# Performance work log

Measured on AMD Instinct MI355X. Metric: run time of the kernel, lower is better.

Reference implementation:

```python
import jax, jax.numpy as jnp
import numpy as np

H, DH = 16, 64  # heads, dim_head; inner = H*DH = 1024
EPS = 1e-5


def _ln(t, g, b):
    mu = jnp.mean(t, axis=-1, keepdims=True)
    var = jnp.var(t, axis=-1, keepdims=True)
    return (t - mu) * jax.lax.rsqrt(var + EPS) * g + b


def _split_heads(t):
    b, n, _ = t.shape
    return t.reshape(b, n, H, DH).transpose(0, 2, 1, 3)  # (b,h,n,dh)


def setup_inputs() -> dict:
    key = jax.random.key(0)
    ks = jax.random.split(key, 5)
    B, S, M, D = 16, 64, 4096, 1024  # S must equal DH (see source einsum quirk)
    return {
        "x": jax.random.normal(ks[0], (B, S, D), jnp.float32),
        "latents": jax.random.normal(ks[1], (B, M, D), jnp.float32),
        "ln_x_g": jnp.ones((D,), jnp.float32),
        "ln_x_b": jnp.zeros((D,), jnp.float32),
        "ln_l_g": jnp.ones((D,), jnp.float32),
        "ln_l_b": jnp.zeros((D,), jnp.float32),
        "Wq": jax.random.normal(ks[2], (D, H * DH), jnp.float32) * 0.02,
        "Wkv": jax.random.normal(ks[3], (D, 2 * H * DH), jnp.float32) * 0.02,
        "Wout": jax.random.normal(ks[4], (H * DH, D), jnp.float32) * 0.02,
    }


def reference(x, latents, ln_x_g, ln_x_b, ln_l_g, ln_l_b, Wq, Wkv, Wout):
    scale = DH ** -0.5
    xn = _ln(x, ln_x_g, ln_x_b)          # (B,S,D)
    ln = _ln(latents, ln_l_g, ln_l_b)    # (B,M,D)
    q = _split_heads(ln @ Wq) * scale    # (B,H,M,DH)
    k, v = map(_split_heads, jnp.split(xn @ Wkv, 2, axis=-1))  # (B,H,S,DH)
    sim = jnp.einsum('bhid,bhjd->bhij', q, k)                  # (B,H,M,S)
    sim = sim - jax.lax.stop_gradient(jnp.max(sim, axis=-1, keepdims=True))
    attn = jax.nn.softmax(sim, axis=-1)
    # Faithful to source: einsum('b h i d, b h j d -> b h i j', attn, v)
    # contracts attn's S dim with v's DH dim (requires S == DH); out = attn @ v^T.
    out = jnp.einsum('bhis,bhjs->bhij', attn, v)               # (B,H,M,S)
    b, _, m, _ = out.shape
    out = out.transpose(0, 2, 1, 3).reshape(b, m, H * DH)      # (B,M,inner)
    return out @ Wout                                          # (B,M,D)
```

## Files before the change

### kernel.cpp

```cpp
#include <hip/hip_runtime.h>
#include <stdint.h>

#define B_ 16
#define S_ 64
#define M_ 4096
#define D_ 1024
#define H_ 16
#define DH_ 64

typedef unsigned short ushort_t;
typedef __attribute__((ext_vector_type(8))) __bf16 bfrag;
typedef __attribute__((ext_vector_type(4))) float f32x4;

__device__ __forceinline__ ushort_t f2bf(float f) {
  union { float f; uint32_t u; } v; v.f = f;
  uint32_t r = v.u + 0x7fffu + ((v.u >> 16) & 1u);
  return (ushort_t)(r >> 16);
}

__device__ __forceinline__ void gload_lds16(const void* g, void* l) {
  __builtin_amdgcn_global_load_lds((const __attribute__((address_space(1))) void*)g,
                                   (__attribute__((address_space(3))) void*)l, 16, 0, 0);
}

__device__ __forceinline__ f32x4 mfma16x16x32(bfrag a, bfrag b, f32x4 c) {
  return __builtin_amdgcn_mfma_f32_16x16x32_bf16(a, b, c, 0, 0, 0);
}

__device__ __forceinline__ int fsw(int r) { return (((r >> 2) & 3) << 1) | (r & 1); }

__global__ __launch_bounds__(256) void ln_rows_kernel(
    const float* __restrict__ x, const float* __restrict__ g,
    const float* __restrict__ bta, ushort_t* __restrict__ out) {
  const int row = blockIdx.x;
  const int t = threadIdx.x;
  const float4* xr = (const float4*)(x + (size_t)row * D_);
  float4 v = xr[t];
  float s = v.x + v.y + v.z + v.w;
  float ss = v.x * v.x + v.y * v.y + v.z * v.z + v.w * v.w;
#pragma unroll
  for (int o = 32; o >= 1; o >>= 1) { s += __shfl_down(s, o); ss += __shfl_down(ss, o); }
  __shared__ float red[16];
  const int wid = t >> 6;
  if ((t & 63) == 0) { red[wid] = s; red[8 + wid] = ss; }
  __syncthreads();
  float tot = red[0] + red[1] + red[2] + red[3];
  float tot2 = red[8] + red[9] + red[10] + red[11];
  float mu = tot * (1.0f / D_);
  float var = tot2 * (1.0f / D_) - mu * mu;
  float rstd = rsqrtf(var + 1e-5f);
  float4 gg = ((const float4*)g)[t];
  float4 bb = ((const float4*)bta)[t];
  ushort_t ob[4];
  ob[0] = f2bf((v.x - mu) * rstd * gg.x + bb.x);
  ob[1] = f2bf((v.y - mu) * rstd * gg.y + bb.y);
  ob[2] = f2bf((v.z - mu) * rstd * gg.z + bb.z);
  ob[3] = f2bf((v.w - mu) * rstd * gg.w + bb.w);
  *(uint2*)(out + (size_t)row * D_ + t * 4) = *(const uint2*)ob;
}

__global__ void transpose_cast_kernel(const float* __restrict__ W, ushort_t* __restrict__ WT,
                                      int N, float scale) {
  __shared__ float tile[32][33];
  const int n0 = blockIdx.x * 32, k0 = blockIdx.y * 32;
  const int tx = threadIdx.x, ty = threadIdx.y;
#pragma unroll
  for (int i = ty; i < 32; i += 8)
    tile[i][tx] = W[(size_t)(k0 + i) * N + n0 + tx];
  __syncthreads();
#pragma unroll
  for (int i = ty; i < 32; i += 8)
    WT[(size_t)(n0 + i) * D_ + k0 + tx] = f2bf(tile[tx][i] * scale);
}

__global__ __launch_bounds__(256) void gemm_kv_kernel(
    const ushort_t* __restrict__ A, const ushort_t* __restrict__ Bt,
    ushort_t* __restrict__ kb, ushort_t* __restrict__ vb) {
  __shared__ __align__(16) ushort_t sA[128 * 32];
  __shared__ __align__(16) ushort_t sB[128 * 32];
  const int tid = threadIdx.x, wid = tid >> 6, lane = tid & 63;
  const size_t arow0 = (size_t)blockIdx.x * 128;
  const size_t brow0 = (size_t)blockIdx.y * 128;
  const int wr = (wid >> 1) * 64, wc = (wid & 1) * 64;
  const int srow = tid >> 2, scol = (tid & 3) * 8;
  const ushort_t* ga = A + (arow0 + srow) * (size_t)D_ + scol;
  const ushort_t* gb = Bt + (brow0 + srow) * (size_t)D_ + scol;
  const int frow = lane & 15, kslot = (lane >> 4) * 8;
  f32x4 acc[4][4] = {};
  for (int k0 = 0; k0 < D_; k0 += 32) {
    gload_lds16(ga, sA + wid * 512);
    gload_lds16(ga + 64 * (size_t)D_, sA + 2048 + wid * 512);
    gload_lds16(gb, sB + wid * 512);
    gload_lds16(gb + 64 * (size_t)D_, sB + 2048 + wid * 512);
    ga += 32; gb += 32;
    __syncthreads();
    bfrag af[4], bfv[4];
#pragma unroll
    for (int m = 0; m < 4; ++m)
      af[m] = *(const bfrag*)&sA[(wr + m * 16 + frow) * 32 + kslot];
#pragma unroll
    for (int n = 0; n < 4; ++n)
      bfv[n] = *(const bfrag*)&sB[(wc + n * 16 + frow) * 32 + kslot];
#pragma unroll
    for (int m = 0; m < 4; ++m)
#pragma unroll
      for (int n = 0; n < 4; ++n)
        acc[m][n] = mfma16x16x32(af[m], bfv[n], acc[m][n]);
    __syncthreads();
  }
  const int erow = (lane >> 4) * 4, ecol = lane & 15;
#pragma unroll
  for (int m = 0; m < 4; ++m)
#pragma unroll
    for (int n = 0; n < 4; ++n)
#pragma unroll
      for (int r = 0; r < 4; ++r) {
        size_t i = arow0 + wr + m * 16 + erow + r;
        int bb = (int)(i >> 6), s = (int)(i & 63);
        size_t n2 = brow0 + wc + n * 16 + ecol;
        ushort_t val = f2bf(acc[m][n][r]);
        ushort_t* dst = (n2 < 1024) ? kb : vb;
        size_t hh = (n2 & 1023) >> 6, d = n2 & 63;
        dst[(((size_t)bb * H_ + hh) * S_ + s) * DH_ + d] = val;
      }
}

template <int MODE>
__global__ __launch_bounds__(256, 2) void gemm128_kernel(
    const ushort_t* __restrict__ A, const ushort_t* __restrict__ Bt,
    const ushort_t* __restrict__ kbuf, const ushort_t* __restrict__ vbuf,
    void* __restrict__ Cout) {
  __shared__ __align__(16) ushort_t lds[24576];
  const int tid = threadIdx.x, wid = tid >> 6, lane = tid & 63;
  const int frow = lane & 15, klo = lane >> 4;
  const int wm = wid >> 1, wn = wid & 1;

  const int l = ((int)blockIdx.x & 7) * 256 + ((int)blockIdx.x >> 3);
  const int mblk = l >> 3, nblk = l & 7;
  const size_t arow0 = (size_t)mblk * 256;
  const size_t bcol0 = (size_t)nblk * 128;

  const int r0 = tid >> 2;
  const int gsrc = (tid & 3) ^ ((tid >> 3) & 3);
  const ushort_t* pA = A + (arow0 + r0) * (size_t)D_ + gsrc * 8;
  const ushort_t* pB = Bt + (bcol0 + r0) * (size_t)D_ + gsrc * 8;
  const int rasw = (klo ^ ((frow >> 1) & 3)) * 8;

#define STAGE(G)                                                                   \
  do {                                                                             \
    const int s_ = (G) & 1;                                                        \
    const size_t ko_ = (size_t)((G) < 32 ? (G) : 31) * 32;                         \
    gload_lds16(pA + ko_, &lds[s_ * 8192 + wid * 512]);                            \
    gload_lds16(pA + 64 * (size_t)D_ + ko_, &lds[s_ * 8192 + 2048 + wid * 512]);   \
    gload_lds16(pA + 128 * (size_t)D_ + ko_, &lds[s_ * 8192 + 4096 + wid * 512]);  \
    gload_lds16(pA + 192 * (size_t)D_ + ko_, &lds[s_ * 8192 + 6144 + wid * 512]);  \
    gload_lds16(pB + ko_, &lds[16384 + s_ * 4096 + wid * 512]);                    \
    gload_lds16(pB + 64 * (size_t)D_ + ko_, &lds[16384 + s_ * 4096 + 2048 + wid * 512]); \
  } while (0)

  STAGE(0);
  STAGE(1);

  f32x4 acc[8][4] = {};
  for (int g = 0; g < 32; ++g) {
    asm volatile("s_waitcnt vmcnt(6)" ::: "memory");
    __builtin_amdgcn_s_barrier();
    asm volatile("" ::: "memory");
    const ushort_t* As = &lds[(g & 1) * 8192];
    const ushort_t* Bs = &lds[16384 + (g & 1) * 4096];
    bfrag a_[8], b_[4];
#pragma unroll
    for (int mf = 0; mf < 8; ++mf)
      a_[mf] = *(const bfrag*)&As[(wm * 128 + mf * 16 + frow) * 32 + rasw];
#pragma unroll
    for (int nf = 0; nf < 4; ++nf)
      b_[nf] = *(const bfrag*)&Bs[(wn * 64 + nf * 16 + frow) * 32 + rasw];
    __builtin_amdgcn_s_setprio(1);
#pragma unroll
    for (int mf = 0; mf < 8; ++mf)
#pragma unroll
      for (int nf = 0; nf < 4; ++nf)
        acc[mf][nf] = mfma16x16x32(a_[mf], b_[nf], acc[mf][nf]);
    __builtin_amdgcn_s_setprio(0);
    asm volatile("" ::: "memory");
    __builtin_amdgcn_s_barrier();
    asm volatile("" ::: "memory");
    STAGE(g + 2);
  }
  asm volatile("s_waitcnt vmcnt(0)" ::: "memory");
  __builtin_amdgcn_s_barrier();
  asm volatile("" ::: "memory");
#undef STAGE

  if constexpr (MODE == 0) {
    float* C = (float*)Cout;
#pragma unroll
    for (int m = 0; m < 8; ++m)
#pragma unroll
      for (int n = 0; n < 4; ++n)
#pragma unroll
        for (int r = 0; r < 4; ++r)
          C[(arow0 + wm * 128 + m * 16 + klo * 4 + r) * 1024 + bcol0 + wn * 64 + n * 16 + frow] =
              acc[m][n][r];
  } else {
    ushort_t* W = &lds[wid * 4096];
    ushort_t* out1 = (ushort_t*)Cout;
    const int head = nblk * 2 + wn;
    const int bbatch = mblk >> 4;
    const size_t kvbase = ((size_t)bbatch * H_ + head) * (size_t)(S_ * DH_);
    bfrag kb[4][2], vb[4][2];
#pragma unroll
    for (int nf = 0; nf < 4; ++nf)
#pragma unroll
      for (int kk = 0; kk < 2; ++kk) {
        kb[nf][kk] = *(const bfrag*)&kbuf[kvbase + (nf * 16 + frow) * 64 + kk * 32 + klo * 8];
        vb[nf][kk] = *(const bfrag*)&vbuf[kvbase + (nf * 16 + frow) * 64 + kk * 32 + klo * 8];
      }
#pragma unroll
    for (int hh = 0; hh < 2; ++hh) {
#pragma unroll
      for (int m2 = 0; m2 < 4; ++m2)
#pragma unroll
        for (int r = 0; r < 4; ++r) {
          const int row = m2 * 16 + klo * 4 + r;
          const int fs = fsw(row);
#pragma unroll
          for (int n = 0; n < 4; ++n) {
            const int cc = n * 16 + frow;
            W[row * 64 + ((((cc >> 3) ^ fs) << 3) | (cc & 7))] = f2bf(acc[hh * 4 + m2][n][r]);
          }
        }
      f32x4 s[4][4] = {};
#pragma unroll
      for (int m2 = 0; m2 < 4; ++m2) {
        const int row = m2 * 16 + frow;
        const int fs = fsw(row);
#pragma unroll
        for (int kk = 0; kk < 2; ++kk) {
          bfrag qa = *(const bfrag*)&W[row * 64 + (((kk * 4 + klo) ^ fs) << 3)];
#pragma unroll
          for (int nf = 0; nf < 4; ++nf)
            s[m2][nf] = mfma16x16x32(qa, kb[nf][kk], s[m2][nf]);
        }
      }
#pragma unroll
      for (int m2 = 0; m2 < 4; ++m2)
#pragma unroll
        for (int r = 0; r < 4; ++r) {
          float a0 = s[m2][0][r], a1 = s[m2][1][r], a2 = s[m2][2][r], a3 = s[m2][3][r];
          float mx = fmaxf(fmaxf(a0, a1), fmaxf(a2, a3));
#pragma unroll
          for (int o = 1; o < 16; o <<= 1) mx = fmaxf(mx, __shfl_xor(mx, o));
          a0 = __expf(a0 - mx); a1 = __expf(a1 - mx);
          a2 = __expf(a2 - mx); a3 = __expf(a3 - mx);
          float sm = (a0 + a1) + (a2 + a3);
#pragma unroll
          for (int o = 1; o < 16; o <<= 1) sm += __shfl_xor(sm, o);
          const float inv = 1.0f / sm;
          s[m2][0][r] = a0 * inv; s[m2][1][r] = a1 * inv;
          s[m2][2][r] = a2 * inv; s[m2][3][r] = a3 * inv;
        }
#pragma unroll
      for (int m2 = 0; m2 < 4; ++m2)
#pragma unroll
        for (int r = 0; r < 4; ++r) {
          const int row = m2 * 16 + klo * 4 + r;
          const int fs = fsw(row);
#pragma unroll
          for (int n = 0; n < 4; ++n) {
            const int cc = n * 16 + frow;
            W[row * 64 + ((((cc >> 3) ^ fs) << 3) | (cc & 7))] = f2bf(s[m2][n][r]);
          }
        }
      f32x4 o[4][4] = {};
#pragma unroll
      for (int m2 = 0; m2 < 4; ++m2) {
        const int row = m2 * 16 + frow;
        const int fs = fsw(row);
#pragma unroll
        for (int kk = 0; kk < 2; ++kk) {
          bfrag pa = *(const bfrag*)&W[row * 64 + (((kk * 4 + klo) ^ fs) << 3)];
#pragma unroll
          for (int nf = 0; nf < 4; ++nf)
            o[m2][nf] = mfma16x16x32(pa, vb[nf][kk], o[m2][nf]);
        }
      }
#pragma unroll
      for (int m2 = 0; m2 < 4; ++m2)
#pragma unroll
        for (int r = 0; r < 4; ++r) {
          const int row = m2 * 16 + klo * 4 + r;
          const int fs = fsw(row);
#pragma unroll
          for (int n = 0; n < 4; ++n) {
            const int cc = n * 16 + frow;
            W[row * 64 + ((((cc >> 3) ^ fs) << 3) | (cc & 7))] = f2bf(o[m2][n][r]);
          }
        }
      const size_t grow0 = arow0 + wm * 128 + hh * 64;
#pragma unroll
      for (int it = 0; it < 8; ++it) {
        const int idx = it * 64 + lane;
        const int rr = idx >> 3, gs = idx & 7;
        const int gcol = (gs ^ fsw(rr)) << 3;
        *(uint4*)&out1[(grow0 + rr) * 1024 + head * 64 + gcol] =
            *(const uint4*)&W[rr * 64 + gs * 8];
      }
    }
  }
}

extern "C" void kernel_launch(void* const* d_in, const int* in_sizes, int n_in,
                              void* d_out, int out_size, void* d_ws, size_t ws_size,
                              hipStream_t stream) {
  const float* x = (const float*)d_in[0];
  const float* lat = (const float*)d_in[1];
  const float* lxg = (const float*)d_in[2];
  const float* lxb = (const float*)d_in[3];
  const float* llg = (const float*)d_in[4];
  const float* llb = (const float*)d_in[5];
  const float* Wq = (const float*)d_in[6];
  const float* Wkv = (const float*)d_in[7];
  const float* Wout = (const float*)d_in[8];
  float* out = (float*)d_out;
  char* ws = (char*)d_ws;

  ushort_t* xn = (ushort_t*)(ws);
  ushort_t* wqT = (ushort_t*)(ws + (2ull << 20));
  ushort_t* wkvT = (ushort_t*)(ws + (4ull << 20));
  ushort_t* woT = (ushort_t*)(ws + (8ull << 20));
  ushort_t* kbuf = (ushort_t*)(ws + (10ull << 20));
  ushort_t* vbuf = (ushort_t*)(ws + (12ull << 20));
  ushort_t* out1 = (ushort_t*)(ws + (14ull << 20));
  ushort_t* lnl = (ushort_t*)d_out;

  dim3 tb(32, 8);
  transpose_cast_kernel<<<dim3(1024 / 32, 32), tb, 0, stream>>>(Wq, wqT, 1024, 0.125f);
  transpose_cast_kernel<<<dim3(2048 / 32, 32), tb, 0, stream>>>(Wkv, wkvT, 2048, 1.0f);
  transpose_cast_kernel<<<dim3(1024 / 32, 32), tb, 0, stream>>>(Wout, woT, 1024, 1.0f);
  ln_rows_kernel<<<B_ * S_, 256, 0, stream>>>(x, lxg, lxb, xn);
  ln_rows_kernel<<<B_ * M_, 256, 0, stream>>>(lat, llg, llb, lnl);
  gemm_kv_kernel<<<dim3(8, 16), 256, 0, stream>>>(xn, wkvT, kbuf, vbuf);
  gemm128_kernel<1><<<2048, 256, 0, stream>>>(lnl, wqT, kbuf, vbuf, out1);
  gemm128_kernel<0><<<2048, 256, 0, stream>>>(out1, woT, nullptr, nullptr, out);
}
```

Baseline: 501.3 us.

## Shrink GEMM tiles to 128x128 and drop double-buffered LDS pipeline

Replaces the 256x128 double-buffered GEMM with a 128x128 single-buffered tile, so twice as many blocks launch and launch bounds target 3 blocks per CU. The explicit vmcnt and barrier software pipeline and the setprio hints are replaced by plain load-then-syncthreads iterations. The fused attention epilogue now handles one 64-row slice per wave instead of looping over two. This aims for more occupancy and fewer registers, but gives up load/compute overlap within a block and halves A/B reuse per tile.

Result: slower. 549.9 us (+9.7%).

```diff
diff --git a/kernel.cpp b/kernel.cpp
--- a/kernel.cpp
+++ b/kernel.cpp
@@ -126,186 +126,167 @@
 }
 
 template <int MODE>
-__global__ __launch_bounds__(256, 2) void gemm128_kernel(
+__global__ __launch_bounds__(256, 3) void gemm97_kernel(
     const ushort_t* __restrict__ A, const ushort_t* __restrict__ Bt,
     const ushort_t* __restrict__ kbuf, const ushort_t* __restrict__ vbuf,
     void* __restrict__ Cout) {
   __shared__ __align__(16) ushort_t lds[24576];
+  ushort_t* const sA = lds;
+  ushort_t* const sB = lds + 4096;
   const int tid = threadIdx.x, wid = tid >> 6, lane = tid & 63;
   const int frow = lane & 15, klo = lane >> 4;
-  const int wm = wid >> 1, wn = wid & 1;
-
-  const int l = ((int)blockIdx.x & 7) * 256 + ((int)blockIdx.x >> 3);
+  const int wr = (wid >> 1) * 64, wc = (wid & 1) * 64;
+
+  const int l = ((int)blockIdx.x & 7) * 512 + ((int)blockIdx.x >> 3);
   const int mblk = l >> 3, nblk = l & 7;
-  const size_t arow0 = (size_t)mblk * 256;
+  const size_t arow0 = (size_t)mblk * 128;
   const size_t bcol0 = (size_t)nblk * 128;
 
   const int r0 = tid >> 2;
   const int gsrc = (tid & 3) ^ ((tid >> 3) & 3);
-  const ushort_t* pA = A + (arow0 + r0) * (size_t)D_ + gsrc * 8;
-  const ushort_t* pB = Bt + (bcol0 + r0) * (size_t)D_ + gsrc * 8;
+  const ushort_t* gA = A + (arow0 + r0) * (size_t)D_ + gsrc * 8;
+  const ushort_t* gB = Bt + (bcol0 + r0) * (size_t)D_ + gsrc * 8;
   const int rasw = (klo ^ ((frow >> 1) & 3)) * 8;
 
-#define STAGE(G)                                                                   \
-  do {                                                                             \
-    const int s_ = (G) & 1;                                                        \
-    const size_t ko_ = (size_t)((G) < 32 ? (G) : 31) * 32;                         \
-    gload_lds16(pA + ko_, &lds[s_ * 8192 + wid * 512]);                            \
-    gload_lds16(pA + 64 * (size_t)D_ + ko_, &lds[s_ * 8192 + 2048 + wid * 512]);   \
-    gload_lds16(pA + 128 * (size_t)D_ + ko_, &lds[s_ * 8192 + 4096 + wid * 512]);  \
-    gload_lds16(pA + 192 * (size_t)D_ + ko_, &lds[s_ * 8192 + 6144 + wid * 512]);  \
-    gload_lds16(pB + ko_, &lds[16384 + s_ * 4096 + wid * 512]);                    \
-    gload_lds16(pB + 64 * (size_t)D_ + ko_, &lds[16384 + s_ * 4096 + 2048 + wid * 512]); \
-  } while (0)
-
-  STAGE(0);
-  STAGE(1);
-
-  f32x4 acc[8][4] = {};
-  for (int g = 0; g < 32; ++g) {
-    asm volatile("s_waitcnt vmcnt(6)" ::: "memory");
-    __builtin_amdgcn_s_barrier();
-    asm volatile("" ::: "memory");
-    const ushort_t* As = &lds[(g & 1) * 8192];
-    const ushort_t* Bs = &lds[16384 + (g & 1) * 4096];
-    bfrag a_[8], b_[4];
-#pragma unroll
-    for (int mf = 0; mf < 8; ++mf)
-      a_[mf] = *(const bfrag*)&As[(wm * 128 + mf * 16 + frow) * 32 + rasw];
+  f32x4 acc[4][4] = {};
+  for (int k0 = 0; k0 < 32; ++k0) {
+    gload_lds16(gA, sA + wid * 512);
+    gload_lds16(gA + 64 * (size_t)D_, sA + 2048 + wid * 512);
+    gload_lds16(gB, sB + wid * 512);
+    gload_lds16(gB + 64 * (size_t)D_, sB + 2048 + wid * 512);
+    gA += 32; gB += 32;
+    __syncthreads();
+    bfrag a_[4], b_[4];
+#pragma unroll
+    for (int mf = 0; mf < 4; ++mf)
+      a_[mf] = *(const bfrag*)&sA[(wr + mf * 16 + frow) * 32 + rasw];
 #pragma unroll
     for (int nf = 0; nf < 4; ++nf)
-      b_[nf] = *(const bfrag*)&Bs[(wn * 64 + nf * 16 + frow) * 32 + rasw];
-    __builtin_amdgcn_s_setprio(1);
-#pragma unroll
-    for (int mf = 0; mf < 8; ++mf)
+      b_[nf] = *(const bfrag*)&sB[(wc + nf * 16 + frow) * 32 + rasw];
+#pragma unroll
+    for (int mf = 0; mf < 4; ++mf)
 #pragma unroll
       for (int nf = 0; nf < 4; ++nf)
         acc[mf][nf] = mfma16x16x32(a_[mf], b_[nf], acc[mf][nf]);
-    __builtin_amdgcn_s_setprio(0);
-    asm volatile("" ::: "memory");
-    __builtin_amdgcn_s_barrier();
-    asm volatile("" ::: "memory");
-    STAGE(g + 2);
+    __syncthreads();
   }
-  asm volatile("s_waitcnt vmcnt(0)" ::: "memory");
-  __builtin_amdgcn_s_barrier();
-  asm volatile("" ::: "memory");
-#undef STAGE
 
   if constexpr (MODE == 0) {
     float* C = (float*)Cout;
 #pragma unroll
-    for (int m = 0; m < 8; ++m)
+    for (int m = 0; m < 4; ++m)
 #pragma unroll
       for (int n = 0; n < 4; ++n)
 #pragma unroll
         for (int r = 0; r < 4; ++r)
-          C[(arow0 + wm * 128 + m * 16 + klo * 4 + r) * 1024 + bcol0 + wn * 64 + n * 16 + frow] =
+          C[(arow0 + wr + m * 16 + klo * 4 + r) * 1024 + bcol0 + wc + n * 16 + frow] =
               acc[m][n][r];
   } else {
-    ushort_t* W = &lds[wid * 4096];
+    ushort_t* W = &lds[8192 + wid * 4096];
     ushort_t* out1 = (ushort_t*)Cout;
-    const int head = nblk * 2 + wn;
-    const int bbatch = mblk >> 4;
+    const int head = nblk * 2 + (wid & 1);
+    const int bbatch = mblk >> 5;
     const size_t kvbase = ((size_t)bbatch * H_ + head) * (size_t)(S_ * DH_);
-    bfrag kb[4][2], vb[4][2];
+
+#pragma unroll
+    for (int m2 = 0; m2 < 4; ++m2)
+#pragma unroll
+      for (int r = 0; r < 4; ++r) {
+        const int row = m2 * 16 + klo * 4 + r;
+        const int fs = fsw(row);
+#pragma unroll
+        for (int n = 0; n < 4; ++n) {
+          const int cc = n * 16 + frow;
+          W[row * 64 + ((((cc >> 3) ^ fs) << 3) | (cc & 7))] = f2bf(acc[m2][n][r]);
+        }
+      }
+    bfrag kb[4][2];
 #pragma unroll
     for (int nf = 0; nf < 4; ++nf)
 #pragma unroll
+      for (int kk = 0; kk < 2; ++kk)
+        kb[nf][kk] = *(const bfrag*)&kbuf[kvbase + (nf * 16 + frow) * 64 + kk * 32 + klo * 8];
+    f32x4 s[4][4] = {};
+#pragma unroll
+    for (int m2 = 0; m2 < 4; ++m2) {
+      const int row = m2 * 16 + frow;
+      const int fs = fsw(row);
+#pragma unroll
       for (int kk = 0; kk < 2; ++kk) {
-        kb[nf][kk] = *(const bfrag*)&kbuf[kvbase + (nf * 16 + frow) * 64 + kk * 32 + klo * 8];
+        bfrag qa = *(const bfrag*)&W[row * 64 + (((kk * 4 + klo) ^ fs) << 3)];
+#pragma unroll
+        for (int nf = 0; nf < 4; ++nf)
+          s[m2][nf] = mfma16x16x32(qa, kb[nf][kk], s[m2][nf]);
+      }
+    }
+#pragma unroll
+    for (int m2 = 0; m2 < 4; ++m2)
+#pragma unroll
+      for (int r = 0; r < 4; ++r) {
+        float a0 = s[m2][0][r], a1 = s[m2][1][r], a2 = s[m2][2][r], a3 = s[m2][3][r];
+        float mx = fmaxf(fmaxf(a0, a1), fmaxf(a2, a3));
+#pragma unroll
+        for (int o = 1; o < 16; o <<= 1) mx = fmaxf(mx, __shfl_xor(mx, o));
+        a0 = __expf(a0 - mx); a1 = __expf(a1 - mx);
+        a2 = __expf(a2 - mx); a3 = __expf(a3 - mx);
+        float sm = (a0 + a1) + (a2 + a3);
+#pragma unroll
+        for (int o = 1; o < 16; o <<= 1) sm += __shfl_xor(sm, o);
+        const float inv = 1.0f / sm;
+        s[m2][0][r] = a0 * inv; s[m2][1][r] = a1 * inv;
+        s[m2][2][r] = a2 * inv; s[m2][3][r] = a3 * inv;
+      }
+#pragma unroll
+    for (int m2 = 0; m2 < 4; ++m2)
+#pragma unroll
+      for (int r = 0; r < 4; ++r) {
+        const int row = m2 * 16 + klo * 4 + r;
+        const int fs = fsw(row);
+#pragma unroll
+        for (int n = 0; n < 4; ++n) {
+          const int cc = n * 16 + frow;
+          W[row * 64 + ((((cc >> 3) ^ fs) << 3) | (cc & 7))] = f2bf(s[m2][n][r]);
+        }
+      }
+    bfrag vb[4][2];
+#pragma unroll
+    for (int nf = 0; nf < 4; ++nf)
+#pragma unroll
+      for (int kk = 0; kk < 2; ++kk)
         vb[nf][kk] = *(const bfrag*)&vbuf[kvbase + (nf * 16 + frow) * 64 + kk * 32 + klo * 8];
-      }
-#pragma unroll
-    for (int hh = 0; hh < 2; ++hh) {
-#pragma unroll
-      for (int m2 = 0; m2 < 4; ++m2)
-#pragma unroll
-        for (int r = 0; r < 4; ++r) {
-          const int row = m2 * 16 + klo * 4 + r;
-          const int fs = fsw(row);
-#pragma unroll
-          for (int n = 0; n < 4; ++n) {
-            const int cc = n * 16 + frow;
-            W[row * 64 + ((((cc >> 3) ^ fs) << 3) | (cc & 7))] = f2bf(acc[hh * 4 + m2][n][r]);
-          }
+    f32x4 o[4][4] = {};
+#pragma unroll
+    for (int m2 = 0; m2 < 4; ++m2) {
+      const int row = m2 * 16 + frow;
+      const int fs = fsw(row);
+#pragma unroll
+      for (int kk = 0; kk < 2; ++kk) {
+        bfrag pa = *(const bfrag*)&W[row * 64 + (((kk * 4 + klo) ^ fs) << 3)];
+#pragma unroll
+        for (int nf = 0; nf < 4; ++nf)
+          o[m2][nf] = mfma16x16x32(pa, vb[nf][kk], o[m2][nf]);
+      }
+    }
+#pragma unroll
+    for (int m2 = 0; m2 < 4; ++m2)
+#pragma unroll
+      for (int r = 0; r < 4; ++r) {
+        const int row = m2 * 16 + klo * 4 + r;
+        const int fs = fsw(row);
+#pragma unroll
+        for (int n = 0; n < 4; ++n) {
+          const int cc = n * 16 + frow;
+          W[row * 64 + ((((cc >> 3) ^ fs) << 3) | (cc & 7))] = f2bf(o[m2][n][r]);
         }
-      f32x4 s[4][4] = {};
-#pragma unroll
-      for (int m2 = 0; m2 < 4; ++m2) {
-        const int row = m2 * 16 + frow;
-        const int fs = fsw(row);
-#pragma unroll
-        for (int kk = 0; kk < 2; ++kk) {
-          bfrag qa = *(const bfrag*)&W[row * 64 + (((kk * 4 + klo) ^ fs) << 3)];
-#pragma unroll
-          for (int nf = 0; nf < 4; ++nf)
-            s[m2][nf] = mfma16x16x32(qa, kb[nf][kk], s[m2][nf]);
-        }
-      }
-#pragma unroll
-      for (int m2 = 0; m2 < 4; ++m2)
-#pragma unroll
-        for (int r = 0; r < 4; ++r) {
-          float a0 = s[m2][0][r], a1 = s[m2][1][r], a2 = s[m2][2][r], a3 = s[m2][3][r];
-          float mx = fmaxf(fmaxf(a0, a1), fmaxf(a2, a3));
-#pragma unroll
-          for (int o = 1; o < 16; o <<= 1) mx = fmaxf(mx, __shfl_xor(mx, o));
-          a0 = __expf(a0 - mx); a1 = __expf(a1 - mx);
-          a2 = __expf(a2 - mx); a3 = __expf(a3 - mx);
-          float sm = (a0 + a1) + (a2 + a3);
-#pragma unroll
-          for (int o = 1; o < 16; o <<= 1) sm += __shfl_xor(sm, o);
-          const float inv = 1.0f / sm;
-          s[m2][0][r] = a0 * inv; s[m2][1][r] = a1 * inv;
-          s[m2][2][r] = a2 * inv; s[m2][3][r] = a3 * inv;
-        }
-#pragma unroll
-      for (int m2 = 0; m2 < 4; ++m2)
-#pragma unroll
-        for (int r = 0; r < 4; ++r) {
-          const int row = m2 * 16 + klo * 4 + r;
-          const int fs = fsw(row);
-#pragma unroll
-          for (int n = 0; n < 4; ++n) {
-            const int cc = n * 16 + frow;
-            W[row * 64 + ((((cc >> 3) ^ fs) << 3) | (cc & 7))] = f2bf(s[m2][n][r]);
-          }
-        }
-      f32x4 o[4][4] = {};
-#pragma unroll
-      for (int m2 = 0; m2 < 4; ++m2) {
-        const int row = m2 * 16 + frow;
-        const int fs = fsw(row);
-#pragma unroll
-        for (int kk = 0; kk < 2; ++kk) {
-          bfrag pa = *(const bfrag*)&W[row * 64 + (((kk * 4 + klo) ^ fs) << 3)];
-#pragma unroll
-          for (int nf = 0; nf < 4; ++nf)
-            o[m2][nf] = mfma16x16x32(pa, vb[nf][kk], o[m2][nf]);
-        }
-      }
-#pragma unroll
-      for (int m2 = 0; m2 < 4; ++m2)
-#pragma unroll
-        for (int r = 0; r < 4; ++r) {
-          const int row = m2 * 16 + klo * 4 + r;
-          const int fs = fsw(row);
-#pragma unroll
-          for (int n = 0; n < 4; ++n) {
-            const int cc = n * 16 + frow;
-            W[row * 64 + ((((cc >> 3) ^ fs) << 3) | (cc & 7))] = f2bf(o[m2][n][r]);
-          }
-        }
-      const size_t grow0 = arow0 + wm * 128 + hh * 64;
-#pragma unroll
-      for (int it = 0; it < 8; ++it) {
-        const int idx = it * 64 + lane;
-        const int rr = idx >> 3, gs = idx & 7;
-        const int gcol = (gs ^ fsw(rr)) << 3;
-        *(uint4*)&out1[(grow0 + rr) * 1024 + head * 64 + gcol] =
-            *(const uint4*)&W[rr * 64 + gs * 8];
-      }
+      }
+    const size_t grow0 = arow0 + wr;
+#pragma unroll
+    for (int it = 0; it < 8; ++it) {
+      const int idx = it * 64 + lane;
+      const int rr = idx >> 3, gs = idx & 7;
+      const int gcol = (gs ^ fsw(rr)) << 3;
+      *(uint4*)&out1[(grow0 + rr) * 1024 + head * 64 + gcol] =
+          *(const uint4*)&W[rr * 64 + gs * 8];
     }
   }
 }
@@ -341,6 +322,6 @@
   ln_rows_kernel<<<B_ * S_, 256, 0, stream>>>(x, lxg, lxb, xn);
   ln_rows_kernel<<<B_ * M_, 256, 0, stream>>>(lat, llg, llb, lnl);
   gemm_kv_kernel<<<dim3(8, 16), 256, 0, stream>>>(xn, wkvT, kbuf, vbuf);
-  gemm128_kernel<1><<<2048, 256, 0, stream>>>(lnl, wqT, kbuf, vbuf, out1);
-  gemm128_kernel<0><<<2048, 256, 0, stream>>>(out1, woT, nullptr, nullptr, out);
-}
+  gemm97_kernel<1><<<4096, 256, 0, stream>>>(lnl, wqT, kbuf, vbuf, out1);
+  gemm97_kernel<0><<<4096, 256, 0, stream>>>(out1, woT, nullptr, nullptr, out);
+}
```
